# Optimization experiments

Measured on AMD Instinct MI355X. Metric: run time of the kernel, lower is better.

## Reference

```python
import jax, jax.numpy as jnp
import numpy as np

B, S, D, H = 8, 256, 16, 256
NH, DH, L = 8, H // 8, 3
H2, H4, FF = H // 2, H // 4, 2 * H


def _ln(x, g, b, eps=1e-5):
    m = jnp.mean(x, axis=-1, keepdims=True)
    v = jnp.var(x, axis=-1, keepdims=True)
    return (x - m) / jnp.sqrt(v + eps) * g + b


def setup_inputs() -> dict:
    key = jax.random.key(0)
    ks = iter(jax.random.split(key, 32))
    w = lambda *sh: jax.random.normal(next(ks), sh, jnp.float32) * 0.05
    inp = {
        'parts': jax.random.normal(next(ks), (B, S, D), jnp.float32),
        'target_sequence': jax.random.randint(next(ks), (B, S), 0, S),
        # part encoder
        'W_pe1': w(H2, D), 'b_pe1': jnp.zeros((H2,)),
        'W_pe2': w(H2, H2), 'b_pe2': jnp.zeros((H2,)),
        'pos_emb': w(S, H4),
        # transformer encoder (3 layers, stacked)
        'Wqkv': w(L, 3 * H, H), 'bqkv': jnp.zeros((L, 3 * H)),
        'Wo': w(L, H, H), 'bo': jnp.zeros((L, H)),
        'ln1_g': jnp.ones((L, H)), 'ln1_b': jnp.zeros((L, H)),
        'W1f': w(L, FF, H), 'b1f': jnp.zeros((L, FF)),
        'W2f': w(L, H, FF), 'b2f': jnp.zeros((L, H)),
        'ln2_g': jnp.ones((L, H)), 'ln2_b': jnp.zeros((L, H)),
        # LSTM decoder
        'Wih': w(4 * H, H), 'Whh': w(4 * H, H),
        'bih': jnp.zeros((4 * H,)), 'bhh': jnp.zeros((4 * H,)),
        # pointer
        'Wp': w(H, H), 'bp': jnp.zeros((H,)), 'v_ptr': w(H),
    }
    return inp


def reference(parts, target_sequence, W_pe1, b_pe1, W_pe2, b_pe2, pos_emb,
              Wqkv, bqkv, Wo, bo, ln1_g, ln1_b, W1f, b1f, W2f, b2f, ln2_g, ln2_b,
              Wih, Whh, bih, bhh, Wp, bp, v_ptr):
    Bk, Sk = parts.shape[:2]
    # ---- encode_inputs (dropout inactive in eval) ----
    pe = jax.nn.relu(parts @ W_pe1.T + b_pe1) @ W_pe2.T + b_pe2          # [B,S,H/2]
    pos = jnp.broadcast_to(pos_emb[None, :Sk], (Bk, Sk, H4))              # [B,S,H/4]
    pad = jnp.zeros((Bk, Sk, H - H2 - H4), parts.dtype)
    x = jnp.concatenate([pe, pos, pad], axis=-1)                          # [B,S,H]
    scale = 1.0 / np.sqrt(DH)
    for l in range(L):  # post-norm transformer encoder layers
        qkv = x @ Wqkv[l].T + bqkv[l]
        q, k, v = jnp.split(qkv, 3, axis=-1)
        q = q.reshape(Bk, Sk, NH, DH)
        k = k.reshape(Bk, Sk, NH, DH)
        v = v.reshape(Bk, Sk, NH, DH)
        att = jax.nn.softmax(jnp.einsum('bqhd,bkhd->bhqk', q, k) * scale, axis=-1)
        o = jnp.einsum('bhqk,bkhd->bqhd', att, v).reshape(Bk, Sk, H)
        o = o @ Wo[l].T + bo[l]
        x = _ln(x + o, ln1_g[l], ln1_b[l])
        f = jax.nn.relu(x @ W1f[l].T + b1f[l]) @ W2f[l].T + b2f[l]
        x = _ln(x + f, ln2_g[l], ln2_b[l])
    enc = x                                                               # [B,S,H]
    # ---- teacher-forced LSTM decode (teacher_forcing_ratio=1.0) ----
    gathered = jnp.take_along_axis(enc, target_sequence[:, :, None], axis=1)  # [B,T,H]
    dec_in = jnp.concatenate([jnp.zeros((Bk, 1, H), enc.dtype), gathered[:, :-1]], 1)
    dec_in = dec_in.transpose(1, 0, 2)                                    # [T,B,H]

    def step(carry, xt):
        h, c = carry
        g = xt @ Wih.T + bih + h @ Whh.T + bhh
        i, f, gg, o = jnp.split(g, 4, axis=-1)
        c = jax.nn.sigmoid(f) * c + jax.nn.sigmoid(i) * jnp.tanh(gg)
        h = jax.nn.sigmoid(o) * jnp.tanh(c)
        return (h, c), h

    h0 = jnp.zeros((Bk, H), enc.dtype)
    _, dec_out = jax.lax.scan(step, (h0, h0), dec_in)
    dec_out = dec_out.transpose(1, 0, 2)                                  # [B,T,H]
    # ---- pointer logits: v . tanh(Wp d_t + Wp e_i), batched over (t,i) ----
    pd = dec_out @ Wp.T + bp                                              # [B,T,H]
    pen = enc @ Wp.T + bp                                                 # [B,S,H]
    logits = jnp.tanh(pd[:, :, None, :] + pen[:, None, :, :]) @ v_ptr     # [B,T,S]
    return logits
```

## Files before the change

kernel.cpp:

```cpp
#include <hip/hip_runtime.h>
#include <cstdint>
#include <cstddef>

typedef _Float16 h2 __attribute__((ext_vector_type(2)));
typedef short bf16x8 __attribute__((ext_vector_type(8)));
typedef float f32x4 __attribute__((ext_vector_type(4)));

__device__ __forceinline__ float sigf(float x) { return 1.0f / (1.0f + __expf(-x)); }
__device__ __forceinline__ float tanhfast(float x) {
  float e = __expf(-2.0f * fabsf(x));
  float t = (1.0f - e) / (1.0f + e);
  return copysignf(t, x);
}
__device__ __forceinline__ h2 cvt2(float a, float b) {
  h2 r; r.x = (_Float16)a; r.y = (_Float16)b; return r;
}
__device__ __forceinline__ h2 bch2(unsigned int u) { return __builtin_bit_cast(h2, u); }
__device__ __forceinline__ unsigned int bcu(h2 v) { return __builtin_bit_cast(unsigned int, v); }
__device__ __forceinline__ unsigned short f2bf(float f) {
  unsigned int u = __float_as_uint(f);
  u = (u + 0x7fffu + ((u >> 16) & 1u)) >> 16;
  return (unsigned short)u;
}

__device__ __forceinline__ float fdot2f(h2 a, h2 b, float c) {
#if __has_builtin(__builtin_amdgcn_fdot2)
  return __builtin_amdgcn_fdot2(a, b, c, false);
#else
  return fmaf((float)a.x, (float)b.x, fmaf((float)a.y, (float)b.y, c));
#endif
}

__global__ void convert_bf(const float* __restrict__ src, ushort* __restrict__ dst, int n) {
  int i = blockIdx.x * 256 + threadIdx.x;
  if (i < n) dst[i] = f2bf(src[i]);
}

__global__ void part_encoder(const float* __restrict__ parts, const float* __restrict__ Wpe1,
                             const float* __restrict__ bpe1, const float* __restrict__ Wpe2,
                             const float* __restrict__ bpe2, const float* __restrict__ pos,
                             float* __restrict__ x, ushort* __restrict__ xb) {
  __shared__ float prow[16];
  __shared__ float pe1[128];
  int row = blockIdx.x;
  int s = row & 255;
  int tid = threadIdx.x;
  if (tid < 16) prow[tid] = parts[row * 16 + tid];
  __syncthreads();
  float a = bpe1[tid];
#pragma unroll
  for (int k = 0; k < 16; ++k) a = fmaf(prow[k], Wpe1[tid * 16 + k], a);
  pe1[tid] = fmaxf(a, 0.0f);
  __syncthreads();
  float a2 = bpe2[tid];
  for (int k = 0; k < 128; ++k) a2 = fmaf(pe1[k], Wpe2[tid * 128 + k], a2);
  x[(size_t)row * 256 + tid] = a2;
  xb[(size_t)row * 256 + tid] = f2bf(a2);
  if (tid < 64) {
    float p = pos[s * 64 + tid];
    x[(size_t)row * 256 + 128 + tid] = p;
    xb[(size_t)row * 256 + 128 + tid] = f2bf(p);
    x[(size_t)row * 256 + 192 + tid] = 0.0f;
    xb[(size_t)row * 256 + 192 + tid] = 0;
  }
}

template <int ACT, int OUTBF>
__global__ __launch_bounds__(256) void gemm_bf16(
    const ushort* __restrict__ A, const ushort* __restrict__ Wt,
    const float* __restrict__ bias1, const float* __restrict__ bias2,
    void* __restrict__ Cout, int N, int K) {
  int wid = threadIdx.x >> 6;
  int lane = threadIdx.x & 63;
  int m0 = blockIdx.y * 64 + wid * 16;
  int n0 = blockIdx.x * 64;
  int r15 = lane & 15;
  int kg = lane >> 4;
  f32x4 acc0 = {0.f, 0.f, 0.f, 0.f}, acc1 = acc0, acc2 = acc0, acc3 = acc0;
  const ushort* arow = A + (size_t)(m0 + r15) * K + kg * 8;
  const ushort* w0 = Wt + (size_t)(n0 + r15) * K + kg * 8;
  const ushort* w1 = w0 + (size_t)16 * K;
  const ushort* w2 = w0 + (size_t)32 * K;
  const ushort* w3 = w0 + (size_t)48 * K;
  for (int k0 = 0; k0 < K; k0 += 32) {
    bf16x8 af = *(const bf16x8*)(arow + k0);
    bf16x8 b0 = *(const bf16x8*)(w0 + k0);
    bf16x8 b1 = *(const bf16x8*)(w1 + k0);
    bf16x8 b2 = *(const bf16x8*)(w2 + k0);
    bf16x8 b3 = *(const bf16x8*)(w3 + k0);
    acc0 = __builtin_amdgcn_mfma_f32_16x16x32_bf16(af, b0, acc0, 0, 0, 0);
    acc1 = __builtin_amdgcn_mfma_f32_16x16x32_bf16(af, b1, acc1, 0, 0, 0);
    acc2 = __builtin_amdgcn_mfma_f32_16x16x32_bf16(af, b2, acc2, 0, 0, 0);
    acc3 = __builtin_amdgcn_mfma_f32_16x16x32_bf16(af, b3, acc3, 0, 0, 0);
  }
#pragma unroll
  for (int nn = 0; nn < 4; ++nn) {
    f32x4 a = (nn == 0) ? acc0 : (nn == 1) ? acc1 : (nn == 2) ? acc2 : acc3;
    int n = n0 + nn * 16 + r15;
    float bsum = bias1[n] + (bias2 ? bias2[n] : 0.0f);
#pragma unroll
    for (int r = 0; r < 4; ++r) {
      int m = m0 + kg * 4 + r;
      float v = a[r] + bsum;
      if (ACT == 1) v = fmaxf(v, 0.0f);
      if (OUTBF == 1)
        ((ushort*)Cout)[(size_t)m * N + n] = f2bf(v);
      else
        ((float*)Cout)[(size_t)m * N + n] = v;
    }
  }
}

__global__ void attn_kernel(const float* __restrict__ qkv, ushort* __restrict__ attout) {
  extern __shared__ float sm[];
  float* kl = sm;
  float* ql = sm + 256 * 33;
  float* sc = sm + 256 * 33 + 32 * 33;
  int qt = blockIdx.x, h = blockIdx.y, b = blockIdx.z;
  int tid = threadIdx.x;
  {
    int j = tid;
    const float* src = qkv + (size_t)(b * 256 + j) * 768 + 256 + h * 32;
#pragma unroll
    for (int d = 0; d < 32; d += 4) {
      float4 v = *(const float4*)(src + d);
      kl[j * 33 + d] = v.x; kl[j * 33 + d + 1] = v.y; kl[j * 33 + d + 2] = v.z; kl[j * 33 + d + 3] = v.w;
    }
  }
  {
    int i = tid >> 3, d4 = (tid & 7) * 4;
    const float* src = qkv + (size_t)(b * 256 + qt * 32 + i) * 768 + h * 32;
    float4 v = *(const float4*)(src + d4);
    ql[i * 33 + d4] = v.x; ql[i * 33 + d4 + 1] = v.y; ql[i * 33 + d4 + 2] = v.z; ql[i * 33 + d4 + 3] = v.w;
  }
  __syncthreads();
  int i = tid >> 3, c = tid & 7;
  const float scale = 0.17677669529663687f;
  float sv[32];
  float mx = -1e30f;
  for (int jj = 0; jj < 32; ++jj) {
    int j = jj * 8 + c;
    float s = 0.0f;
#pragma unroll
    for (int d = 0; d < 32; ++d) s = fmaf(ql[i * 33 + d], kl[j * 33 + d], s);
    s *= scale;
    sv[jj] = s;
    mx = fmaxf(mx, s);
  }
  mx = fmaxf(mx, __shfl_xor(mx, 1));
  mx = fmaxf(mx, __shfl_xor(mx, 2));
  mx = fmaxf(mx, __shfl_xor(mx, 4));
  float sum = 0.0f;
  for (int jj = 0; jj < 32; ++jj) {
    float p = __expf(sv[jj] - mx);
    sc[i * 257 + jj * 8 + c] = p;
    sum += p;
  }
  sum += __shfl_xor(sum, 1);
  sum += __shfl_xor(sum, 2);
  sum += __shfl_xor(sum, 4);
  float inv = 1.0f / sum;
  __syncthreads();
  float a0 = 0, a1 = 0, a2 = 0, a3 = 0;
  int d0 = c * 4;
  const float* vbase = qkv + 512 + h * 32 + d0;
  for (int j = 0; j < 256; ++j) {
    float p = sc[i * 257 + j];
    float4 v = *(const float4*)(vbase + (size_t)(b * 256 + j) * 768);
    a0 = fmaf(p, v.x, a0); a1 = fmaf(p, v.y, a1); a2 = fmaf(p, v.z, a2); a3 = fmaf(p, v.w, a3);
  }
  int orow = b * 256 + qt * 32 + i;
  ushort4 o4;
  o4.x = f2bf(a0 * inv); o4.y = f2bf(a1 * inv); o4.z = f2bf(a2 * inv); o4.w = f2bf(a3 * inv);
  *(ushort4*)&attout[(size_t)orow * 256 + h * 32 + d0] = o4;
}

__global__ void ln_residual(float* __restrict__ x, const float* __restrict__ o,
                            const float* __restrict__ g, const float* __restrict__ bt,
                            ushort* __restrict__ xb) {
  int row = blockIdx.x, tid = threadIdx.x;
  float e = x[(size_t)row * 256 + tid] + o[(size_t)row * 256 + tid];
  float s = e, q = e * e;
#pragma unroll
  for (int off = 32; off >= 1; off >>= 1) {
    s += __shfl_xor(s, off);
    q += __shfl_xor(q, off);
  }
  __shared__ float ps[4], pq[4];
  int wid = tid >> 6, lane = tid & 63;
  if (lane == 0) { ps[wid] = s; pq[wid] = q; }
  __syncthreads();
  float St = ps[0] + ps[1] + ps[2] + ps[3];
  float Qt = pq[0] + pq[1] + pq[2] + pq[3];
  float mean = St * (1.0f / 256.0f);
  float var = Qt * (1.0f / 256.0f) - mean * mean;
  float y = (e - mean) * rsqrtf(var + 1e-5f) * g[tid] + bt[tid];
  x[(size_t)row * 256 + tid] = y;
  xb[(size_t)row * 256 + tid] = f2bf(y);
}

__global__ void gather_dec_in(const ushort* __restrict__ encb, const int* __restrict__ ts,
                              ushort* __restrict__ dec_in) {
  int bx = blockIdx.x;
  int t = bx >> 3, b = bx & 7;
  int tid = threadIdx.x;
  ushort4 v = {0, 0, 0, 0};
  if (t > 0) {
    int sidx = ts[b * 256 + t - 1];
    v = *(const ushort4*)&encb[((size_t)(b * 256 + sidx)) * 256 + tid * 4];
  }
  *(ushort4*)&dec_in[(size_t)bx * 256 + tid * 4] = v;
}

__global__ __attribute__((amdgpu_flat_work_group_size(512, 512), amdgpu_waves_per_eu(1, 1)))
void lstm_scan(const float* __restrict__ Xw, const float* __restrict__ Whh,
               ushort* __restrict__ dec_out) {
  extern __shared__ char smem[];
  uint4* wlds = (uint4*)smem;
  h2* hbuf = (h2*)(smem + 131072);
  int b = blockIdx.x;
  int t0 = threadIdx.x;
  int u = t0 >> 1, p = t0 & 1;
  int rA = u + 256 * p;
  int rB = u + 512 + 256 * p;

  h2 w0[96], w1[96];
  {
    const float4* sA = (const float4*)(Whh + (size_t)rA * 256);
    const float4* sB = (const float4*)(Whh + (size_t)rB * 256);
#pragma unroll
    for (int k = 0; k < 48; ++k) {
      float4 v = sA[k];
      w0[2 * k] = cvt2(v.x, v.y);
      w0[2 * k + 1] = cvt2(v.z, v.w);
    }
#pragma unroll
    for (int k = 0; k < 48; ++k) {
      float4 v = sB[k];
      w1[2 * k] = cvt2(v.x, v.y);
      w1[2 * k + 1] = cvt2(v.z, v.w);
    }
#pragma unroll
    for (int qc = 0; qc < 8; ++qc) {
      float4 vA0 = sA[48 + 2 * qc], vA1 = sA[48 + 2 * qc + 1];
      float4 vB0 = sB[48 + 2 * qc], vB1 = sB[48 + 2 * qc + 1];
      uint4 uA, uB;
      uA.x = bcu(cvt2(vA0.x, vA0.y)); uA.y = bcu(cvt2(vA0.z, vA0.w));
      uA.z = bcu(cvt2(vA1.x, vA1.y)); uA.w = bcu(cvt2(vA1.z, vA1.w));
      uB.x = bcu(cvt2(vB0.x, vB0.y)); uB.y = bcu(cvt2(vB0.z, vB0.w));
      uB.z = bcu(cvt2(vB1.x, vB1.y)); uB.w = bcu(cvt2(vB1.z, vB1.w));
      wlds[qc * 1024 + rA] = uA;
      wlds[qc * 1024 + rB] = uB;
    }
  }
  if (t0 < 128) ((uint4*)hbuf)[t0 & 63] = make_uint4(0, 0, 0, 0);
  float c = 0.0f;
  float xnA = Xw[(size_t)b * 1024 + rA];
  float xnB = Xw[(size_t)b * 1024 + rB];
  __syncthreads();

  for (int t = 0; t < 256; ++t) {
    float xwA = xnA, xwB = xnB;
    if (t < 255) {
      const float* xp = Xw + (size_t)((t + 1) * 8 + b) * 1024;
      xnA = xp[rA]; xnB = xp[rB];
    }
    const uint4* hb = (const uint4*)(hbuf + (size_t)(t & 1) * 128);
    float a0 = 0.0f, a1 = 0.0f;
#pragma unroll
    for (int q = 0; q < 24; ++q) {
      uint4 hv = hb[q];
      h2 hx = bch2(hv.x), hy = bch2(hv.y), hz = bch2(hv.z), hw = bch2(hv.w);
      a0 = fdot2f(w0[4 * q], hx, a0); a0 = fdot2f(w0[4 * q + 1], hy, a0);
      a0 = fdot2f(w0[4 * q + 2], hz, a0); a0 = fdot2f(w0[4 * q + 3], hw, a0);
      a1 = fdot2f(w1[4 * q], hx, a1); a1 = fdot2f(w1[4 * q + 1], hy, a1);
      a1 = fdot2f(w1[4 * q + 2], hz, a1); a1 = fdot2f(w1[4 * q + 3], hw, a1);
    }
#pragma unroll
    for (int qc = 0; qc < 8; ++qc) {
      uint4 hv = hb[24 + qc];
      h2 hx = bch2(hv.x), hy = bch2(hv.y), hz = bch2(hv.z), hw = bch2(hv.w);
      uint4 uA = wlds[qc * 1024 + rA];
      uint4 uB = wlds[qc * 1024 + rB];
      a0 = fdot2f(bch2(uA.x), hx, a0); a0 = fdot2f(bch2(uA.y), hy, a0);
      a0 = fdot2f(bch2(uA.z), hz, a0); a0 = fdot2f(bch2(uA.w), hw, a0);
      a1 = fdot2f(bch2(uB.x), hx, a1); a1 = fdot2f(bch2(uB.y), hy, a1);
      a1 = fdot2f(bch2(uB.z), hz, a1); a1 = fdot2f(bch2(uB.w), hw, a1);
    }
    a0 += xwA;
    a1 += xwB;
    float ev = sigf(a0) * tanhfast(a1);
    float ep = __shfl_xor(ev, 1);
    if (p == 1) {
      c = sigf(a0) * c + ep;
      float hv_ = sigf(a1) * tanhfast(c);
      ((_Float16*)(hbuf + (size_t)((t + 1) & 1) * 128))[u] = (_Float16)hv_;
      dec_out[((size_t)(b * 256 + t)) * 256 + u] = f2bf(hv_);
    }
    __syncthreads();
  }
}

__global__ void transpose_pen(const float* __restrict__ pen, float* __restrict__ penT) {
  int bx = blockIdx.x;
  int b = bx >> 8, h = bx & 255;
  int i = threadIdx.x;
  penT[(size_t)bx * 256 + i] = pen[((size_t)(b * 256 + i)) * 256 + h];
}

__global__ void pointer_kernel(const float* __restrict__ pd, const float* __restrict__ penT,
                               const float* __restrict__ vptr, float* __restrict__ out) {
  __shared__ float pdr[256];
  __shared__ float vl[256];
  int bx = blockIdx.x;
  int b = bx >> 8;
  int tid = threadIdx.x;
  pdr[tid] = pd[(size_t)bx * 256 + tid];
  vl[tid] = vptr[tid];
  __syncthreads();
  const float* pT = penT + (size_t)b * 256 * 256;
  float acc = 0.0f;
  for (int h = 0; h < 256; ++h) {
    acc = fmaf(vl[h], tanhfast(pdr[h] + pT[(size_t)h * 256 + tid]), acc);
  }
  out[(size_t)bx * 256 + tid] = acc;
}

extern "C" void kernel_launch(void* const* d_in, const int* in_sizes, int n_in,
                              void* d_out, int out_size, void* d_ws, size_t ws_size,
                              hipStream_t stream) {
  const float* parts = (const float*)d_in[0];
  const int* ts = (const int*)d_in[1];
  const float* Wpe1 = (const float*)d_in[2];
  const float* bpe1 = (const float*)d_in[3];
  const float* Wpe2 = (const float*)d_in[4];
  const float* bpe2 = (const float*)d_in[5];
  const float* pos = (const float*)d_in[6];
  const float* Wqkv = (const float*)d_in[7];
  const float* bqkv = (const float*)d_in[8];
  const float* Wo = (const float*)d_in[9];
  const float* bo = (const float*)d_in[10];
  const float* ln1g = (const float*)d_in[11];
  const float* ln1b = (const float*)d_in[12];
  const float* W1f = (const float*)d_in[13];
  const float* b1f = (const float*)d_in[14];
  const float* W2f = (const float*)d_in[15];
  const float* b2f = (const float*)d_in[16];
  const float* ln2g = (const float*)d_in[17];
  const float* ln2b = (const float*)d_in[18];
  const float* Wih = (const float*)d_in[19];
  const float* Whh = (const float*)d_in[20];
  const float* bih = (const float*)d_in[21];
  const float* bhh = (const float*)d_in[22];
  const float* Wp = (const float*)d_in[23];
  const float* bp = (const float*)d_in[24];
  const float* vptr = (const float*)d_in[25];
  float* out = (float*)d_out;

  float* W = (float*)d_ws;
  float* xbuf = W;
  ushort* xbf = (ushort*)(W + 524288);
  float* SCR = W + 786432;
  float* qkvb = SCR;
  float* obuf = SCR + 1572864;
  float* Xw = SCR;
  float* pdb = SCR;
  float* penb = SCR + 524288;
  float* penTb = SCR + 1048576;
  ushort* attbf = (ushort*)(W + 2883584);
  ushort* ffbf = (ushort*)(W + 3145728);
  ushort* dec_inbf = (ushort*)(W + 3145728);
  ushort* dec_outbf = (ushort*)(W + 3407872);
  ushort* wqkvbf = (ushort*)(W + 3670016);
  ushort* wobf   = (ushort*)(W + 3964928);
  ushort* w1fbf  = (ushort*)(W + 4063232);
  ushort* w2fbf  = (ushort*)(W + 4259840);
  ushort* wihbf  = (ushort*)(W + 4456448);
  ushort* wpbf   = (ushort*)(W + 4587520);

  const int attnLDS = (256 * 33 + 32 * 33 + 32 * 257) * 4;
  const int scanLDS = 131072 + 1024;
  hipFuncSetAttribute((const void*)attn_kernel, hipFuncAttributeMaxDynamicSharedMemorySize, attnLDS);
  hipFuncSetAttribute((const void*)lstm_scan, hipFuncAttributeMaxDynamicSharedMemorySize, scanLDS);

  convert_bf<<<(589824 + 255) / 256, 256, 0, stream>>>(Wqkv, wqkvbf, 589824);
  convert_bf<<<(196608 + 255) / 256, 256, 0, stream>>>(Wo, wobf, 196608);
  convert_bf<<<(393216 + 255) / 256, 256, 0, stream>>>(W1f, w1fbf, 393216);
  convert_bf<<<(393216 + 255) / 256, 256, 0, stream>>>(W2f, w2fbf, 393216);
  convert_bf<<<(262144 + 255) / 256, 256, 0, stream>>>(Wih, wihbf, 262144);
  convert_bf<<<(65536 + 255) / 256, 256, 0, stream>>>(Wp, wpbf, 65536);

  part_encoder<<<2048, 128, 0, stream>>>(parts, Wpe1, bpe1, Wpe2, bpe2, pos, xbuf, xbf);
  for (int l = 0; l < 3; ++l) {
    gemm_bf16<0, 0><<<dim3(12, 32), 256, 0, stream>>>(xbf, wqkvbf + (size_t)l * 196608,
                                                      bqkv + l * 768, nullptr, qkvb, 768, 256);
    attn_kernel<<<dim3(8, 8, 8), 256, attnLDS, stream>>>(qkvb, attbf);
    gemm_bf16<0, 0><<<dim3(4, 32), 256, 0, stream>>>(attbf, wobf + (size_t)l * 65536,
                                                     bo + l * 256, nullptr, obuf, 256, 256);
    ln_residual<<<2048, 256, 0, stream>>>(xbuf, obuf, ln1g + l * 256, ln1b + l * 256, xbf);
    gemm_bf16<1, 1><<<dim3(8, 32), 256, 0, stream>>>(xbf, w1fbf + (size_t)l * 131072,
                                                     b1f + l * 512, nullptr, ffbf, 512, 256);
    gemm_bf16<0, 0><<<dim3(4, 32), 256, 0, stream>>>(ffbf, w2fbf + (size_t)l * 131072,
                                                     b2f + l * 256, nullptr, obuf, 256, 512);
    ln_residual<<<2048, 256, 0, stream>>>(xbuf, obuf, ln2g + l * 256, ln2b + l * 256, xbf);
  }
  gather_dec_in<<<2048, 64, 0, stream>>>(xbf, ts, dec_inbf);
  gemm_bf16<0, 0><<<dim3(16, 32), 256, 0, stream>>>(dec_inbf, wihbf, bih, bhh, Xw, 1024, 256);
  lstm_scan<<<8, 512, scanLDS, stream>>>(Xw, Whh, dec_outbf);
  gemm_bf16<0, 0><<<dim3(4, 32), 256, 0, stream>>>(dec_outbf, wpbf, bp, nullptr, pdb, 256, 256);
  gemm_bf16<0, 0><<<dim3(4, 32), 256, 0, stream>>>(xbf, wpbf, bp, nullptr, penb, 256, 256);
  transpose_pen<<<2048, 256, 0, stream>>>(penb, penTb);
  pointer_kernel<<<2048, 256, 0, stream>>>(pdb, penTb, vptr, out);
}
```

Baseline: 863.2 us.

## Rewrite LSTM scan as single-block MFMA recurrence over all batches

The LSTM recurrence moves from 8 blocks of per-thread fp16 dot products (one block per batch row) to one 512-thread block that computes all batch rows together with bf16 MFMA. Whh is pre-converted to bf16; part of it is held in registers and the rest in swizzled LDS, and h is double-buffered in LDS. The input projection is now written transposed in bf16 so each step can read it with vector loads. The cost is that the whole 256-step serial chain runs on a single CU, and h, gate inputs and weights lose precision by moving from fp16/fp32 to bf16.

```diff
diff --git a/kernel.cpp b/kernel.cpp
--- a/kernel.cpp
+++ b/kernel.cpp
@@ -2,7 +2,6 @@
 #include <cstdint>
 #include <cstddef>
 
-typedef _Float16 h2 __attribute__((ext_vector_type(2)));
 typedef short bf16x8 __attribute__((ext_vector_type(8)));
 typedef float f32x4 __attribute__((ext_vector_type(4)));
 
@@ -12,23 +11,13 @@
   float t = (1.0f - e) / (1.0f + e);
   return copysignf(t, x);
 }
-__device__ __forceinline__ h2 cvt2(float a, float b) {
-  h2 r; r.x = (_Float16)a; r.y = (_Float16)b; return r;
-}
-__device__ __forceinline__ h2 bch2(unsigned int u) { return __builtin_bit_cast(h2, u); }
-__device__ __forceinline__ unsigned int bcu(h2 v) { return __builtin_bit_cast(unsigned int, v); }
 __device__ __forceinline__ unsigned short f2bf(float f) {
   unsigned int u = __float_as_uint(f);
   u = (u + 0x7fffu + ((u >> 16) & 1u)) >> 16;
   return (unsigned short)u;
 }
-
-__device__ __forceinline__ float fdot2f(h2 a, h2 b, float c) {
-#if __has_builtin(__builtin_amdgcn_fdot2)
-  return __builtin_amdgcn_fdot2(a, b, c, false);
-#else
-  return fmaf((float)a.x, (float)b.x, fmaf((float)a.y, (float)b.y, c));
-#endif
+__device__ __forceinline__ float bfh(unsigned short u) {
+  return __uint_as_float(((unsigned int)u) << 16);
 }
 
 __global__ void convert_bf(const float* __restrict__ src, ushort* __restrict__ dst, int n) {
@@ -65,7 +54,7 @@
   }
 }
 
-template <int ACT, int OUTBF>
+template <int ACT, int OUT>
 __global__ __launch_bounds__(256) void gemm_bf16(
     const ushort* __restrict__ A, const ushort* __restrict__ Wt,
     const float* __restrict__ bias1, const float* __restrict__ bias2,
@@ -98,15 +87,22 @@
     f32x4 a = (nn == 0) ? acc0 : (nn == 1) ? acc1 : (nn == 2) ? acc2 : acc3;
     int n = n0 + nn * 16 + r15;
     float bsum = bias1[n] + (bias2 ? bias2[n] : 0.0f);
-#pragma unroll
-    for (int r = 0; r < 4; ++r) {
-      int m = m0 + kg * 4 + r;
-      float v = a[r] + bsum;
-      if (ACT == 1) v = fmaxf(v, 0.0f);
-      if (OUTBF == 1)
-        ((ushort*)Cout)[(size_t)m * N + n] = f2bf(v);
-      else
-        ((float*)Cout)[(size_t)m * N + n] = v;
+    if (OUT == 2) {
+      ushort4 s;
+      float v0 = a[0] + bsum, v1 = a[1] + bsum, v2 = a[2] + bsum, v3 = a[3] + bsum;
+      s.x = f2bf(v0); s.y = f2bf(v1); s.z = f2bf(v2); s.w = f2bf(v3);
+      *(ushort4*)&((ushort*)Cout)[(size_t)n * 2056 + m0 + kg * 4] = s;
+    } else {
+#pragma unroll
+      for (int r = 0; r < 4; ++r) {
+        int m = m0 + kg * 4 + r;
+        float v = a[r] + bsum;
+        if (ACT == 1) v = fmaxf(v, 0.0f);
+        if (OUT == 1)
+          ((ushort*)Cout)[(size_t)m * N + n] = f2bf(v);
+        else
+          ((float*)Cout)[(size_t)m * N + n] = v;
+      }
     }
   }
 }
@@ -212,92 +208,115 @@
   *(ushort4*)&dec_in[(size_t)bx * 256 + tid * 4] = v;
 }
 
-__global__ __attribute__((amdgpu_flat_work_group_size(512, 512), amdgpu_waves_per_eu(1, 1)))
-void lstm_scan(const float* __restrict__ Xw, const float* __restrict__ Whh,
-               ushort* __restrict__ dec_out) {
+__global__ __launch_bounds__(512) void lstm_scan(
+    const ushort* __restrict__ XwT,
+    const ushort* __restrict__ Whb,
+    ushort* __restrict__ dec_out) {
   extern __shared__ char smem[];
-  uint4* wlds = (uint4*)smem;
-  h2* hbuf = (h2*)(smem + 131072);
-  int b = blockIdx.x;
-  int t0 = threadIdx.x;
-  int u = t0 >> 1, p = t0 & 1;
-  int rA = u + 256 * p;
-  int rB = u + 512 + 256 * p;
-
-  h2 w0[96], w1[96];
-  {
-    const float4* sA = (const float4*)(Whh + (size_t)rA * 256);
-    const float4* sB = (const float4*)(Whh + (size_t)rB * 256);
-#pragma unroll
-    for (int k = 0; k < 48; ++k) {
-      float4 v = sA[k];
-      w0[2 * k] = cvt2(v.x, v.y);
-      w0[2 * k + 1] = cvt2(v.z, v.w);
+  uint4* Bl = (uint4*)smem;
+  uint4* Hl = (uint4*)(smem + 131072);
+  int tid = threadIdx.x;
+  int w = tid >> 6, l = tid & 63;
+  int r15 = l & 15, kg = l >> 4;
+
+  for (int i = 0; i < 16; ++i) {
+    int idx = tid + i * 512;
+    int bw = idx >> 10, lc = (idx >> 5) & 31, oct = idx & 31;
+    int col = 768 + bw * 32 + lc;
+    Bl[bw * 1024 + lc * 32 + (oct ^ (lc & 7))] = ((const uint4*)Whb)[col * 32 + oct];
+  }
+  uint4 z = {0, 0, 0, 0};
+  Hl[tid] = z;
+  Hl[tid + 512] = z;
+
+  bf16x8 fr[48];
+#pragma unroll
+  for (int nt = 0; nt < 6; ++nt) {
+    int g = nt >> 1, hf = nt & 1;
+    int col = g * 256 + w * 32 + hf * 16 + r15;
+#pragma unroll
+    for (int ks = 0; ks < 8; ++ks)
+      fr[nt * 8 + ks] = ((const bf16x8*)Whb)[col * 32 + ks * 4 + kg];
+  }
+  float cst[4] = {0.f, 0.f, 0.f, 0.f};
+  const int hfo = (kg >= 2) ? 1 : 0;
+  const int b0 = (kg & 1) * 4;
+  const int ucol = w * 32 + hfo * 16 + r15;
+  const int lcb = r15;
+  __syncthreads();
+
+  int cur = 0;
+  for (int t = 0; t < 256; ++t) {
+    f32x4 ac0 = {0.f, 0.f, 0.f, 0.f}, ac1 = ac0, ac2 = ac0, ac3 = ac0;
+    f32x4 ac4 = ac0, ac5 = ac0, ac6 = ac0, ac7 = ac0;
+    const uint4* hb = Hl + cur * 512;
+#pragma unroll
+    for (int half = 0; half < 2; ++half) {
+      bf16x8 a0, a1, a2, a3;
+      {
+        int o0 = ((half * 4 + 0) * 4 + kg) ^ (r15 & 7);
+        int o1 = ((half * 4 + 1) * 4 + kg) ^ (r15 & 7);
+        int o2 = ((half * 4 + 2) * 4 + kg) ^ (r15 & 7);
+        int o3 = ((half * 4 + 3) * 4 + kg) ^ (r15 & 7);
+        a0 = ((const bf16x8*)hb)[r15 * 32 + o0];
+        a1 = ((const bf16x8*)hb)[r15 * 32 + o1];
+        a2 = ((const bf16x8*)hb)[r15 * 32 + o2];
+        a3 = ((const bf16x8*)hb)[r15 * 32 + o3];
+      }
+#pragma unroll
+      for (int j = 0; j < 4; ++j) {
+        int ks = half * 4 + j;
+        bf16x8 av = (j == 0) ? a0 : (j == 1) ? a1 : (j == 2) ? a2 : a3;
+        int lc6 = 0 * 16 + lcb, lc7 = 1 * 16 + lcb;
+        bf16x8 b6 = ((const bf16x8*)Bl)[w * 1024 + lc6 * 32 + ((ks * 4 + kg) ^ (lc6 & 7))];
+        bf16x8 b7 = ((const bf16x8*)Bl)[w * 1024 + lc7 * 32 + ((ks * 4 + kg) ^ (lc7 & 7))];
+        ac0 = __builtin_amdgcn_mfma_f32_16x16x32_bf16(av, fr[0 * 8 + ks], ac0, 0, 0, 0);
+        ac1 = __builtin_amdgcn_mfma_f32_16x16x32_bf16(av, fr[1 * 8 + ks], ac1, 0, 0, 0);
+        ac2 = __builtin_amdgcn_mfma_f32_16x16x32_bf16(av, fr[2 * 8 + ks], ac2, 0, 0, 0);
+        ac3 = __builtin_amdgcn_mfma_f32_16x16x32_bf16(av, fr[3 * 8 + ks], ac3, 0, 0, 0);
+        ac4 = __builtin_amdgcn_mfma_f32_16x16x32_bf16(av, fr[4 * 8 + ks], ac4, 0, 0, 0);
+        ac5 = __builtin_amdgcn_mfma_f32_16x16x32_bf16(av, fr[5 * 8 + ks], ac5, 0, 0, 0);
+        ac6 = __builtin_amdgcn_mfma_f32_16x16x32_bf16(av, b6, ac6, 0, 0, 0);
+        ac7 = __builtin_amdgcn_mfma_f32_16x16x32_bf16(av, b7, ac7, 0, 0, 0);
+      }
     }
-#pragma unroll
-    for (int k = 0; k < 48; ++k) {
-      float4 v = sB[k];
-      w1[2 * k] = cvt2(v.x, v.y);
-      w1[2 * k + 1] = cvt2(v.z, v.w);
+    float gv0[4], gv1[4], gv2[4], gv3[4];
+#pragma unroll
+    for (int r = 0; r < 4; ++r) {
+      float s0 = __shfl_xor(ac1[r], 32);
+      float s1 = __shfl_xor(ac3[r], 32);
+      float s2 = __shfl_xor(ac5[r], 32);
+      float s3 = __shfl_xor(ac7[r], 32);
+      gv0[r] = hfo ? s0 : ac0[r];
+      gv1[r] = hfo ? s1 : ac2[r];
+      gv2[r] = hfo ? s2 : ac4[r];
+      gv3[r] = hfo ? s3 : ac6[r];
     }
-#pragma unroll
-    for (int qc = 0; qc < 8; ++qc) {
-      float4 vA0 = sA[48 + 2 * qc], vA1 = sA[48 + 2 * qc + 1];
-      float4 vB0 = sB[48 + 2 * qc], vB1 = sB[48 + 2 * qc + 1];
-      uint4 uA, uB;
-      uA.x = bcu(cvt2(vA0.x, vA0.y)); uA.y = bcu(cvt2(vA0.z, vA0.w));
-      uA.z = bcu(cvt2(vA1.x, vA1.y)); uA.w = bcu(cvt2(vA1.z, vA1.w));
-      uB.x = bcu(cvt2(vB0.x, vB0.y)); uB.y = bcu(cvt2(vB0.z, vB0.w));
-      uB.z = bcu(cvt2(vB1.x, vB1.y)); uB.w = bcu(cvt2(vB1.z, vB1.w));
-      wlds[qc * 1024 + rA] = uA;
-      wlds[qc * 1024 + rB] = uB;
-    }
-  }
-  if (t0 < 128) ((uint4*)hbuf)[t0 & 63] = make_uint4(0, 0, 0, 0);
-  float c = 0.0f;
-  float xnA = Xw[(size_t)b * 1024 + rA];
-  float xnB = Xw[(size_t)b * 1024 + rB];
-  __syncthreads();
-
-  for (int t = 0; t < 256; ++t) {
-    float xwA = xnA, xwB = xnB;
-    if (t < 255) {
-      const float* xp = Xw + (size_t)((t + 1) * 8 + b) * 1024;
-      xnA = xp[rA]; xnB = xp[rB];
-    }
-    const uint4* hb = (const uint4*)(hbuf + (size_t)(t & 1) * 128);
-    float a0 = 0.0f, a1 = 0.0f;
-#pragma unroll
-    for (int q = 0; q < 24; ++q) {
-      uint4 hv = hb[q];
-      h2 hx = bch2(hv.x), hy = bch2(hv.y), hz = bch2(hv.z), hw = bch2(hv.w);
-      a0 = fdot2f(w0[4 * q], hx, a0); a0 = fdot2f(w0[4 * q + 1], hy, a0);
-      a0 = fdot2f(w0[4 * q + 2], hz, a0); a0 = fdot2f(w0[4 * q + 3], hw, a0);
-      a1 = fdot2f(w1[4 * q], hx, a1); a1 = fdot2f(w1[4 * q + 1], hy, a1);
-      a1 = fdot2f(w1[4 * q + 2], hz, a1); a1 = fdot2f(w1[4 * q + 3], hw, a1);
-    }
-#pragma unroll
-    for (int qc = 0; qc < 8; ++qc) {
-      uint4 hv = hb[24 + qc];
-      h2 hx = bch2(hv.x), hy = bch2(hv.y), hz = bch2(hv.z), hw = bch2(hv.w);
-      uint4 uA = wlds[qc * 1024 + rA];
-      uint4 uB = wlds[qc * 1024 + rB];
-      a0 = fdot2f(bch2(uA.x), hx, a0); a0 = fdot2f(bch2(uA.y), hy, a0);
-      a0 = fdot2f(bch2(uA.z), hz, a0); a0 = fdot2f(bch2(uA.w), hw, a0);
-      a1 = fdot2f(bch2(uB.x), hx, a1); a1 = fdot2f(bch2(uB.y), hy, a1);
-      a1 = fdot2f(bch2(uB.z), hz, a1); a1 = fdot2f(bch2(uB.w), hw, a1);
-    }
-    a0 += xwA;
-    a1 += xwB;
-    float ev = sigf(a0) * tanhfast(a1);
-    float ep = __shfl_xor(ev, 1);
-    if (p == 1) {
-      c = sigf(a0) * c + ep;
-      float hv_ = sigf(a1) * tanhfast(c);
-      ((_Float16*)(hbuf + (size_t)((t + 1) & 1) * 128))[u] = (_Float16)hv_;
-      dec_out[((size_t)(b * 256 + t)) * 256 + u] = f2bf(hv_);
+    int tb = t * 8 + b0;
+    ushort4 x0 = *(const ushort4*)&XwT[(size_t)(0 * 256 + ucol) * 2056 + tb];
+    ushort4 x1 = *(const ushort4*)&XwT[(size_t)(1 * 256 + ucol) * 2056 + tb];
+    ushort4 x2 = *(const ushort4*)&XwT[(size_t)(2 * 256 + ucol) * 2056 + tb];
+    ushort4 x3 = *(const ushort4*)&XwT[(size_t)(3 * 256 + ucol) * 2056 + tb];
+    const ushort* px0 = (const ushort*)&x0;
+    const ushort* px1 = (const ushort*)&x1;
+    const ushort* px2 = (const ushort*)&x2;
+    const ushort* px3 = (const ushort*)&x3;
+    ushort* hn = (ushort*)(Hl + (cur ^ 1) * 512);
+#pragma unroll
+    for (int r = 0; r < 4; ++r) {
+      float gi = gv0[r] + bfh(px0[r]);
+      float gf = gv1[r] + bfh(px1[r]);
+      float gg = gv2[r] + bfh(px2[r]);
+      float go = gv3[r] + bfh(px3[r]);
+      float cn = sigf(gf) * cst[r] + sigf(gi) * tanhfast(gg);
+      cst[r] = cn;
+      float hv = sigf(go) * tanhfast(cn);
+      int row = b0 + r;
+      hn[row * 256 + (((ucol >> 3) ^ (row & 7)) * 8) + (ucol & 7)] = f2bf(hv);
+      dec_out[((size_t)(row * 256 + t)) * 256 + ucol] = f2bf(hv);
     }
     __syncthreads();
+    cur ^= 1;
   }
 }
 
@@ -363,7 +382,7 @@
   float* SCR = W + 786432;
   float* qkvb = SCR;
   float* obuf = SCR + 1572864;
-  float* Xw = SCR;
+  ushort* XwT = (ushort*)SCR;
   float* pdb = SCR;
   float* penb = SCR + 524288;
   float* penTb = SCR + 1048576;
@@ -377,9 +396,10 @@
   ushort* w2fbf  = (ushort*)(W + 4259840);
   ushort* wihbf  = (ushort*)(W + 4456448);
   ushort* wpbf   = (ushort*)(W + 4587520);
+  ushort* whhbf  = (ushort*)(W + 4620288);
 
   const int attnLDS = (256 * 33 + 32 * 33 + 32 * 257) * 4;
-  const int scanLDS = 131072 + 1024;
+  const int scanLDS = 131072 + 16384;
   hipFuncSetAttribute((const void*)attn_kernel, hipFuncAttributeMaxDynamicSharedMemorySize, attnLDS);
   hipFuncSetAttribute((const void*)lstm_scan, hipFuncAttributeMaxDynamicSharedMemorySize, scanLDS);
 
@@ -389,6 +409,7 @@
   convert_bf<<<(393216 + 255) / 256, 256, 0, stream>>>(W2f, w2fbf, 393216);
   convert_bf<<<(262144 + 255) / 256, 256, 0, stream>>>(Wih, wihbf, 262144);
   convert_bf<<<(65536 + 255) / 256, 256, 0, stream>>>(Wp, wpbf, 65536);
+  convert_bf<<<(262144 + 255) / 256, 256, 0, stream>>>(Whh, whhbf, 262144);
 
   part_encoder<<<2048, 128, 0, stream>>>(parts, Wpe1, bpe1, Wpe2, bpe2, pos, xbuf, xbf);
   for (int l = 0; l < 3; ++l) {
@@ -405,8 +426,8 @@
     ln_residual<<<2048, 256, 0, stream>>>(xbuf, obuf, ln2g + l * 256, ln2b + l * 256, xbf);
   }
   gather_dec_in<<<2048, 64, 0, stream>>>(xbf, ts, dec_inbf);
-  gemm_bf16<0, 0><<<dim3(16, 32), 256, 0, stream>>>(dec_inbf, wihbf, bih, bhh, Xw, 1024, 256);
-  lstm_scan<<<8, 512, scanLDS, stream>>>(Xw, Whh, dec_outbf);
+  gemm_bf16<0, 2><<<dim3(16, 32), 256, 0, stream>>>(dec_inbf, wihbf, bih, bhh, XwT, 1024, 256);
+  lstm_scan<<<1, 512, scanLDS, stream>>>(XwT, whhbf, dec_outbf);
   gemm_bf16<0, 0><<<dim3(4, 32), 256, 0, stream>>>(dec_outbf, wpbf, bp, nullptr, pdb, 256, 256);
   gemm_bf16<0, 0><<<dim3(4, 32), 256, 0, stream>>>(xbf, wpbf, bp, nullptr, penb, 256, 256);
   transpose_pen<<<2048, 256, 0, stream>>>(penb, penTb);
```

New measurement: 1.504 ms. 1.74x slower.

## Split LSTM scan across four blocks per batch with global flag synchronization

Applied to the files above, without the earlier changes.

The LSTM recurrence for each batch element is spread over four workgroups, 32 blocks in total, instead of one 512-thread block per batch. Each thread now keeps a full Whh row in registers as fp16, so no weights are read from LDS. Each step, the blocks publish their slice of h to global memory and spin on per-block flags with acquire loads to collect the peers' slices. This removes the LDS weight traffic and per-thread compute from the serial path, at the cost of a cross-CU global handshake on every one of the 256 steps, and it assumes all 32 blocks are resident at once.

```diff
diff --git a/kernel.cpp b/kernel.cpp
--- a/kernel.cpp
+++ b/kernel.cpp
@@ -16,7 +16,6 @@
   h2 r; r.x = (_Float16)a; r.y = (_Float16)b; return r;
 }
 __device__ __forceinline__ h2 bch2(unsigned int u) { return __builtin_bit_cast(h2, u); }
-__device__ __forceinline__ unsigned int bcu(h2 v) { return __builtin_bit_cast(unsigned int, v); }
 __device__ __forceinline__ unsigned short f2bf(float f) {
   unsigned int u = __float_as_uint(f);
   u = (u + 0x7fffu + ((u >> 16) & 1u)) >> 16;
@@ -65,7 +64,7 @@
   }
 }
 
-template <int ACT, int OUTBF>
+template <int ACT, int OUT>
 __global__ __launch_bounds__(256) void gemm_bf16(
     const ushort* __restrict__ A, const ushort* __restrict__ Wt,
     const float* __restrict__ bias1, const float* __restrict__ bias2,
@@ -103,7 +102,7 @@
       int m = m0 + kg * 4 + r;
       float v = a[r] + bsum;
       if (ACT == 1) v = fmaxf(v, 0.0f);
-      if (OUTBF == 1)
+      if (OUT == 1)
         ((ushort*)Cout)[(size_t)m * N + n] = f2bf(v);
       else
         ((float*)Cout)[(size_t)m * N + n] = v;
@@ -212,92 +211,83 @@
   *(ushort4*)&dec_in[(size_t)bx * 256 + tid * 4] = v;
 }
 
-__global__ __attribute__((amdgpu_flat_work_group_size(512, 512), amdgpu_waves_per_eu(1, 1)))
+__global__ __attribute__((amdgpu_flat_work_group_size(256, 256), amdgpu_waves_per_eu(1, 1)))
 void lstm_scan(const float* __restrict__ Xw, const float* __restrict__ Whh,
-               ushort* __restrict__ dec_out) {
-  extern __shared__ char smem[];
-  uint4* wlds = (uint4*)smem;
-  h2* hbuf = (h2*)(smem + 131072);
-  int b = blockIdx.x;
-  int t0 = threadIdx.x;
-  int u = t0 >> 1, p = t0 & 1;
-  int rA = u + 256 * p;
-  int rB = u + 512 + 256 * p;
-
-  h2 w0[96], w1[96];
+               ushort* __restrict__ dec_out, unsigned int* __restrict__ hg,
+               unsigned int* __restrict__ flags) {
+  __shared__ _Float16 hbuf[2][256];
+  int bx = blockIdx.x;
+  int s4 = bx >> 3, b = bx & 7;
+  int tid = threadIdx.x;
+  int ul = tid >> 2, g = tid & 3;
+  int gu = s4 * 64 + ul;
+  int R = g * 256 + gu;
+
+  h2 w[128];
   {
-    const float4* sA = (const float4*)(Whh + (size_t)rA * 256);
-    const float4* sB = (const float4*)(Whh + (size_t)rB * 256);
-#pragma unroll
-    for (int k = 0; k < 48; ++k) {
-      float4 v = sA[k];
-      w0[2 * k] = cvt2(v.x, v.y);
-      w0[2 * k + 1] = cvt2(v.z, v.w);
-    }
-#pragma unroll
-    for (int k = 0; k < 48; ++k) {
-      float4 v = sB[k];
-      w1[2 * k] = cvt2(v.x, v.y);
-      w1[2 * k + 1] = cvt2(v.z, v.w);
-    }
-#pragma unroll
-    for (int qc = 0; qc < 8; ++qc) {
-      float4 vA0 = sA[48 + 2 * qc], vA1 = sA[48 + 2 * qc + 1];
-      float4 vB0 = sB[48 + 2 * qc], vB1 = sB[48 + 2 * qc + 1];
-      uint4 uA, uB;
-      uA.x = bcu(cvt2(vA0.x, vA0.y)); uA.y = bcu(cvt2(vA0.z, vA0.w));
-      uA.z = bcu(cvt2(vA1.x, vA1.y)); uA.w = bcu(cvt2(vA1.z, vA1.w));
-      uB.x = bcu(cvt2(vB0.x, vB0.y)); uB.y = bcu(cvt2(vB0.z, vB0.w));
-      uB.z = bcu(cvt2(vB1.x, vB1.y)); uB.w = bcu(cvt2(vB1.z, vB1.w));
-      wlds[qc * 1024 + rA] = uA;
-      wlds[qc * 1024 + rB] = uB;
-    }
-  }
-  if (t0 < 128) ((uint4*)hbuf)[t0 & 63] = make_uint4(0, 0, 0, 0);
+    const float4* src = (const float4*)(Whh + (size_t)R * 256);
+#pragma unroll
+    for (int k = 0; k < 64; ++k) {
+      float4 v = src[k];
+      w[2 * k] = cvt2(v.x, v.y);
+      w[2 * k + 1] = cvt2(v.z, v.w);
+    }
+  }
+  hbuf[0][tid] = (_Float16)0.0f;
   float c = 0.0f;
-  float xnA = Xw[(size_t)b * 1024 + rA];
-  float xnB = Xw[(size_t)b * 1024 + rB];
-  __syncthreads();
-
+  float xnext = Xw[(size_t)b * 1024 + R];
+  unsigned int* myflag = &flags[bx];
+  int lw = tid & 63, qbase = lw & ~3;
+  __syncthreads();
+
+  int cur = 0;
   for (int t = 0; t < 256; ++t) {
-    float xwA = xnA, xwB = xnB;
+    float xcur = xnext;
+    if (t < 255) xnext = Xw[(size_t)((t + 1) * 8 + b) * 1024 + R];
+    const uint4* hb = (const uint4*)hbuf[cur];
+    float a0 = 0.f, a1 = 0.f, a2 = 0.f, a3 = 0.f;
+#pragma unroll
+    for (int q = 0; q < 32; ++q) {
+      uint4 hv = hb[q];
+      a0 = fdot2f(w[4 * q + 0], bch2(hv.x), a0);
+      a1 = fdot2f(w[4 * q + 1], bch2(hv.y), a1);
+      a2 = fdot2f(w[4 * q + 2], bch2(hv.z), a2);
+      a3 = fdot2f(w[4 * q + 3], bch2(hv.w), a3);
+    }
+    float gsum = (a0 + a1) + (a2 + a3) + xcur;
+    float gi = __shfl(gsum, qbase + 0);
+    float gf = __shfl(gsum, qbase + 1);
+    float gg = __shfl(gsum, qbase + 2);
+    float go = __shfl(gsum, qbase + 3);
+    c = sigf(gf) * c + sigf(gi) * tanhfast(gg);
+    float hv_ = sigf(go) * tanhfast(c);
+    _Float16 hf = (_Float16)hv_;
+    if (g == 0) hbuf[cur ^ 1][gu] = hf;
+    if (g == 1 && t < 255) {
+      __hip_atomic_store(&hg[(size_t)((t + 1) & 1) * 2048 + b * 256 + gu],
+                         (unsigned int)__builtin_bit_cast(unsigned short, hf),
+                         __ATOMIC_RELAXED, __HIP_MEMORY_SCOPE_AGENT);
+    }
+    if (g == 2) dec_out[((size_t)(b * 256 + t)) * 256 + gu] = f2bf(hv_);
     if (t < 255) {
-      const float* xp = Xw + (size_t)((t + 1) * 8 + b) * 1024;
-      xnA = xp[rA]; xnB = xp[rB];
-    }
-    const uint4* hb = (const uint4*)(hbuf + (size_t)(t & 1) * 128);
-    float a0 = 0.0f, a1 = 0.0f;
-#pragma unroll
-    for (int q = 0; q < 24; ++q) {
-      uint4 hv = hb[q];
-      h2 hx = bch2(hv.x), hy = bch2(hv.y), hz = bch2(hv.z), hw = bch2(hv.w);
-      a0 = fdot2f(w0[4 * q], hx, a0); a0 = fdot2f(w0[4 * q + 1], hy, a0);
-      a0 = fdot2f(w0[4 * q + 2], hz, a0); a0 = fdot2f(w0[4 * q + 3], hw, a0);
-      a1 = fdot2f(w1[4 * q], hx, a1); a1 = fdot2f(w1[4 * q + 1], hy, a1);
-      a1 = fdot2f(w1[4 * q + 2], hz, a1); a1 = fdot2f(w1[4 * q + 3], hw, a1);
-    }
-#pragma unroll
-    for (int qc = 0; qc < 8; ++qc) {
-      uint4 hv = hb[24 + qc];
-      h2 hx = bch2(hv.x), hy = bch2(hv.y), hz = bch2(hv.z), hw = bch2(hv.w);
-      uint4 uA = wlds[qc * 1024 + rA];
-      uint4 uB = wlds[qc * 1024 + rB];
-      a0 = fdot2f(bch2(uA.x), hx, a0); a0 = fdot2f(bch2(uA.y), hy, a0);
-      a0 = fdot2f(bch2(uA.z), hz, a0); a0 = fdot2f(bch2(uA.w), hw, a0);
-      a1 = fdot2f(bch2(uB.x), hx, a1); a1 = fdot2f(bch2(uB.y), hy, a1);
-      a1 = fdot2f(bch2(uB.z), hz, a1); a1 = fdot2f(bch2(uB.w), hw, a1);
-    }
-    a0 += xwA;
-    a1 += xwB;
-    float ev = sigf(a0) * tanhfast(a1);
-    float ep = __shfl_xor(ev, 1);
-    if (p == 1) {
-      c = sigf(a0) * c + ep;
-      float hv_ = sigf(a1) * tanhfast(c);
-      ((_Float16*)(hbuf + (size_t)((t + 1) & 1) * 128))[u] = (_Float16)hv_;
-      dec_out[((size_t)(b * 256 + t)) * 256 + u] = f2bf(hv_);
-    }
-    __syncthreads();
+      __syncthreads();
+      if (tid == 0)
+        __hip_atomic_fetch_add(myflag, 1u, __ATOMIC_RELAXED, __HIP_MEMORY_SCOPE_AGENT);
+      if (tid < 192) {
+        int pi = tid >> 6;
+        int p = pi + (pi >= s4 ? 1 : 0);
+        unsigned int* pf = &flags[p * 8 + b];
+        while (__hip_atomic_load(pf, __ATOMIC_ACQUIRE, __HIP_MEMORY_SCOPE_AGENT) <= (unsigned)t)
+          __builtin_amdgcn_s_sleep(1);
+        int u2 = tid & 63;
+        unsigned int v = __hip_atomic_load(
+            &hg[(size_t)((t + 1) & 1) * 2048 + b * 256 + p * 64 + u2],
+            __ATOMIC_RELAXED, __HIP_MEMORY_SCOPE_AGENT);
+        hbuf[cur ^ 1][p * 64 + u2] = __builtin_bit_cast(_Float16, (unsigned short)v);
+      }
+      __syncthreads();
+    }
+    cur ^= 1;
   }
 }
 
@@ -377,11 +367,11 @@
   ushort* w2fbf  = (ushort*)(W + 4259840);
   ushort* wihbf  = (ushort*)(W + 4456448);
   ushort* wpbf   = (ushort*)(W + 4587520);
+  unsigned int* hg = (unsigned int*)(W + 4620288);
+  unsigned int* flags = (unsigned int*)(W + 4624384);
 
   const int attnLDS = (256 * 33 + 32 * 33 + 32 * 257) * 4;
-  const int scanLDS = 131072 + 1024;
   hipFuncSetAttribute((const void*)attn_kernel, hipFuncAttributeMaxDynamicSharedMemorySize, attnLDS);
-  hipFuncSetAttribute((const void*)lstm_scan, hipFuncAttributeMaxDynamicSharedMemorySize, scanLDS);
 
   convert_bf<<<(589824 + 255) / 256, 256, 0, stream>>>(Wqkv, wqkvbf, 589824);
   convert_bf<<<(196608 + 255) / 256, 256, 0, stream>>>(Wo, wobf, 196608);
@@ -406,7 +396,8 @@
   }
   gather_dec_in<<<2048, 64, 0, stream>>>(xbf, ts, dec_inbf);
   gemm_bf16<0, 0><<<dim3(16, 32), 256, 0, stream>>>(dec_inbf, wihbf, bih, bhh, Xw, 1024, 256);
-  lstm_scan<<<8, 512, scanLDS, stream>>>(Xw, Whh, dec_outbf);
+  hipMemsetAsync(flags, 0, 32 * sizeof(unsigned int), stream);
+  lstm_scan<<<32, 256, 0, stream>>>(Xw, Whh, dec_outbf, hg, flags);
   gemm_bf16<0, 0><<<dim3(4, 32), 256, 0, stream>>>(dec_outbf, wpbf, bp, nullptr, pdb, 256, 256);
   gemm_bf16<0, 0><<<dim3(4, 32), 256, 0, stream>>>(xbf, wpbf, bp, nullptr, penb, 256, 256);
   transpose_pen<<<2048, 256, 0, stream>>>(penb, penTb);
```

Result: slower. 1.158 ms (+34.2%).

## Add 1024-thread LSTM scan and fuse pen transpose into GEMM epilogue

Applied to the files above, without the earlier changes.

Adds a new LSTM scan kernel that uses 1024 threads, one per gate row. Each thread holds most of its Whh row in registers and the rest in LDS, and gate values are exchanged through shared memory before 256 threads update the cell state. A host-side check on register count and spills picks between the new and old scan. The pen GEMM also writes its output transposed directly, through a new epilogue mode, which removes the separate transpose kernel and its extra memory round trip. The new scan adds a second barrier per timestep, and whether it runs depends on the compiler's register allocation.

```diff
diff --git a/kernel.cpp b/kernel.cpp
--- a/kernel.cpp
+++ b/kernel.cpp
@@ -65,7 +65,7 @@
   }
 }
 
-template <int ACT, int OUTBF>
+template <int ACT, int OUT>
 __global__ __launch_bounds__(256) void gemm_bf16(
     const ushort* __restrict__ A, const ushort* __restrict__ Wt,
     const float* __restrict__ bias1, const float* __restrict__ bias2,
@@ -98,15 +98,22 @@
     f32x4 a = (nn == 0) ? acc0 : (nn == 1) ? acc1 : (nn == 2) ? acc2 : acc3;
     int n = n0 + nn * 16 + r15;
     float bsum = bias1[n] + (bias2 ? bias2[n] : 0.0f);
-#pragma unroll
-    for (int r = 0; r < 4; ++r) {
-      int m = m0 + kg * 4 + r;
-      float v = a[r] + bsum;
-      if (ACT == 1) v = fmaxf(v, 0.0f);
-      if (OUTBF == 1)
-        ((ushort*)Cout)[(size_t)m * N + n] = f2bf(v);
-      else
-        ((float*)Cout)[(size_t)m * N + n] = v;
+    if (OUT == 3) {
+      int b = m0 >> 8;
+      int mloc = (m0 & 255) + kg * 4;
+      float4 o4 = {a[0] + bsum, a[1] + bsum, a[2] + bsum, a[3] + bsum};
+      *(float4*)&((float*)Cout)[((size_t)(b * 256 + n)) * 256 + mloc] = o4;
+    } else {
+#pragma unroll
+      for (int r = 0; r < 4; ++r) {
+        int m = m0 + kg * 4 + r;
+        float v = a[r] + bsum;
+        if (ACT == 1) v = fmaxf(v, 0.0f);
+        if (OUT == 1)
+          ((ushort*)Cout)[(size_t)m * N + n] = f2bf(v);
+        else
+          ((float*)Cout)[(size_t)m * N + n] = v;
+      }
     }
   }
 }
@@ -212,9 +219,80 @@
   *(ushort4*)&dec_in[(size_t)bx * 256 + tid * 4] = v;
 }
 
+__global__ __attribute__((amdgpu_flat_work_group_size(1024, 1024), amdgpu_waves_per_eu(2)))
+void lstm_scan1024(const float* __restrict__ Xw, const float* __restrict__ Whh,
+                   ushort* __restrict__ dec_out) {
+  extern __shared__ char smem[];
+  uint4* wlds = (uint4*)smem;
+  _Float16* hbuf = (_Float16*)(smem + 131072);
+  float* gp = (float*)(smem + 131072 + 1024);
+  int b = blockIdx.x;
+  int R = threadIdx.x;
+
+  h2 w[96];
+  {
+    const float4* src = (const float4*)(Whh + (size_t)R * 256);
+#pragma unroll
+    for (int k = 0; k < 48; ++k) {
+      float4 v = src[k];
+      w[2 * k] = cvt2(v.x, v.y);
+      w[2 * k + 1] = cvt2(v.z, v.w);
+    }
+#pragma unroll
+    for (int qc = 0; qc < 8; ++qc) {
+      float4 v = src[48 + 2 * qc], v2 = src[48 + 2 * qc + 1];
+      uint4 u;
+      u.x = bcu(cvt2(v.x, v.y));  u.y = bcu(cvt2(v.z, v.w));
+      u.z = bcu(cvt2(v2.x, v2.y)); u.w = bcu(cvt2(v2.z, v2.w));
+      wlds[qc * 1024 + R] = u;
+    }
+  }
+  if (R < 256) { hbuf[R] = (_Float16)0.0f; hbuf[256 + R] = (_Float16)0.0f; }
+  float c = 0.0f;
+  float xnext = Xw[(size_t)b * 1024 + R];
+  __syncthreads();
+
+  int cur = 0;
+  for (int t = 0; t < 256; ++t) {
+    float xcur = xnext;
+    if (t < 255) xnext = Xw[(size_t)((t + 1) * 8 + b) * 1024 + R];
+    const uint4* hb = (const uint4*)(hbuf + cur * 256);
+    float a0 = 0.f, a1 = 0.f, a2 = 0.f, a3 = 0.f;
+#pragma unroll
+    for (int q = 0; q < 24; ++q) {
+      uint4 hv = hb[q];
+      a0 = fdot2f(w[4 * q + 0], bch2(hv.x), a0);
+      a1 = fdot2f(w[4 * q + 1], bch2(hv.y), a1);
+      a2 = fdot2f(w[4 * q + 2], bch2(hv.z), a2);
+      a3 = fdot2f(w[4 * q + 3], bch2(hv.w), a3);
+    }
+#pragma unroll
+    for (int qc = 0; qc < 8; ++qc) {
+      uint4 hv = hb[24 + qc];
+      uint4 wv = wlds[qc * 1024 + R];
+      a0 = fdot2f(bch2(wv.x), bch2(hv.x), a0);
+      a1 = fdot2f(bch2(wv.y), bch2(hv.y), a1);
+      a2 = fdot2f(bch2(wv.z), bch2(hv.z), a2);
+      a3 = fdot2f(bch2(wv.w), bch2(hv.w), a3);
+    }
+    gp[R] = (a0 + a1) + (a2 + a3) + xcur;
+    __syncthreads();
+    int nxt = cur ^ 1;
+    if (R < 256) {
+      float gi = gp[R], gf = gp[256 + R], gg = gp[512 + R], go = gp[768 + R];
+      c = sigf(gf) * c + sigf(gi) * tanhfast(gg);
+      float hv_ = sigf(go) * tanhfast(c);
+      hbuf[nxt * 256 + R] = (_Float16)hv_;
+      dec_out[((size_t)(b * 256 + t)) * 256 + R] = f2bf(hv_);
+    }
+    __syncthreads();
+    cur = nxt;
+  }
+}
+
 __global__ __attribute__((amdgpu_flat_work_group_size(512, 512), amdgpu_waves_per_eu(1, 1)))
-void lstm_scan(const float* __restrict__ Xw, const float* __restrict__ Whh,
-               ushort* __restrict__ dec_out) {
+void lstm_scan512(const float* __restrict__ Xw, const float* __restrict__ Whh,
+                  ushort* __restrict__ dec_out) {
   extern __shared__ char smem[];
   uint4* wlds = (uint4*)smem;
   h2* hbuf = (h2*)(smem + 131072);
@@ -299,13 +377,6 @@
     }
     __syncthreads();
   }
-}
-
-__global__ void transpose_pen(const float* __restrict__ pen, float* __restrict__ penT) {
-  int bx = blockIdx.x;
-  int b = bx >> 8, h = bx & 255;
-  int i = threadIdx.x;
-  penT[(size_t)bx * 256 + i] = pen[((size_t)(b * 256 + i)) * 256 + h];
 }
 
 __global__ void pointer_kernel(const float* __restrict__ pd, const float* __restrict__ penT,
@@ -365,7 +436,6 @@
   float* obuf = SCR + 1572864;
   float* Xw = SCR;
   float* pdb = SCR;
-  float* penb = SCR + 524288;
   float* penTb = SCR + 1048576;
   ushort* attbf = (ushort*)(W + 2883584);
   ushort* ffbf = (ushort*)(W + 3145728);
@@ -379,9 +449,16 @@
   ushort* wpbf   = (ushort*)(W + 4587520);
 
   const int attnLDS = (256 * 33 + 32 * 33 + 32 * 257) * 4;
-  const int scanLDS = 131072 + 1024;
+  const int scan512LDS = 131072 + 1024;
+  const int scan1024LDS = 131072 + 1024 + 4096;
   hipFuncSetAttribute((const void*)attn_kernel, hipFuncAttributeMaxDynamicSharedMemorySize, attnLDS);
-  hipFuncSetAttribute((const void*)lstm_scan, hipFuncAttributeMaxDynamicSharedMemorySize, scanLDS);
+  hipFuncSetAttribute((const void*)lstm_scan512, hipFuncAttributeMaxDynamicSharedMemorySize, scan512LDS);
+  hipFuncSetAttribute((const void*)lstm_scan1024, hipFuncAttributeMaxDynamicSharedMemorySize, scan1024LDS);
+
+  hipFuncAttributes fa1024{};
+  bool use1024 = false;
+  if (hipFuncGetAttributes(&fa1024, (const void*)lstm_scan1024) == hipSuccess)
+    use1024 = (fa1024.localSizeBytes == 0 && fa1024.numRegs >= 100);
 
   convert_bf<<<(589824 + 255) / 256, 256, 0, stream>>>(Wqkv, wqkvbf, 589824);
   convert_bf<<<(196608 + 255) / 256, 256, 0, stream>>>(Wo, wobf, 196608);
@@ -406,9 +483,11 @@
   }
   gather_dec_in<<<2048, 64, 0, stream>>>(xbf, ts, dec_inbf);
   gemm_bf16<0, 0><<<dim3(16, 32), 256, 0, stream>>>(dec_inbf, wihbf, bih, bhh, Xw, 1024, 256);
-  lstm_scan<<<8, 512, scanLDS, stream>>>(Xw, Whh, dec_outbf);
+  if (use1024)
+    lstm_scan1024<<<8, 1024, scan1024LDS, stream>>>(Xw, Whh, dec_outbf);
+  else
+    lstm_scan512<<<8, 512, scan512LDS, stream>>>(Xw, Whh, dec_outbf);
   gemm_bf16<0, 0><<<dim3(4, 32), 256, 0, stream>>>(dec_outbf, wpbf, bp, nullptr, pdb, 256, 256);
-  gemm_bf16<0, 0><<<dim3(4, 32), 256, 0, stream>>>(xbf, wpbf, bp, nullptr, penb, 256, 256);
-  transpose_pen<<<2048, 256, 0, stream>>>(penb, penTb);
+  gemm_bf16<0, 3><<<dim3(4, 32), 256, 0, stream>>>(xbf, wpbf, bp, nullptr, penTb, 256, 256);
   pointer_kernel<<<2048, 256, 0, stream>>>(pdb, penTb, vptr, out);
 }
```

Measured after the change: 859.1 us. About the same (-0.5%).
